# Kernel tuning notes

Hardware: AMD Instinct MI355X
Metric: run time of the kernel (lower is better)

## Reference

```python
import jax, jax.numpy as jnp
import numpy as np

N, E, DIN, DH, DP = 100000, 1600000, 128, 128, 64
BN_EPS = 1e-5


def setup_inputs() -> dict:
    key = jax.random.key(0)
    ks = jax.random.split(key, 24)

    def lin(k, fan_in, shape):
        return jax.random.normal(k, shape, jnp.float32) / np.sqrt(fan_in)

    inp = {
        "x": jax.random.normal(ks[0], (N, DIN), jnp.float32),
        "edge_index": jax.random.randint(ks[1], (2, E), 0, N, dtype=jnp.int32),
        "edge_type": jax.random.randint(ks[2], (E,), 0, 2, dtype=jnp.int32),
        "edge_weight": jax.random.uniform(ks[3], (E,), jnp.float32),
        "seed_node_id": 12345,
        # feature transform
        "ft_w": lin(ks[4], DIN, (DIN, DH)),
        "ft_b": jnp.zeros((DH,), jnp.float32),
        # GCN block 0: 2 layers, stacked along axis 0
        "g0_w": lin(ks[5], DH, (2, DH, DH)),
        "g0_b": jnp.zeros((2, DH), jnp.float32),
        "g0_gamma": jnp.ones((2, DH), jnp.float32),
        "g0_beta": jnp.zeros((2, DH), jnp.float32),
        "g0_rm": 0.1 * jax.random.normal(ks[6], (2, DH), jnp.float32),
        "g0_rv": 0.5 + jax.random.uniform(ks[7], (2, DH), jnp.float32),
        # GCN block 1
        "g1_w": lin(ks[8], DH, (2, DH, DH)),
        "g1_b": jnp.zeros((2, DH), jnp.float32),
        "g1_gamma": jnp.ones((2, DH), jnp.float32),
        "g1_beta": jnp.zeros((2, DH), jnp.float32),
        "g1_rm": 0.1 * jax.random.normal(ks[9], (2, DH), jnp.float32),
        "g1_rv": 0.5 + jax.random.uniform(ks[10], (2, DH), jnp.float32),
        # predictor (input = 4*DH)
        "p_w1": lin(ks[11], 4 * DH, (4 * DH, DP)),
        "p_b1": jnp.zeros((DP,), jnp.float32),
        "p_w2": lin(ks[12], DP, (DP, DP)),
        "p_b2": jnp.zeros((DP,), jnp.float32),
        "p_w3": lin(ks[13], DP, (DP, 1)),
        "p_b3": jnp.zeros((1,), jnp.float32),
    }
    return inp


def _gcn_conv(x, src, dst, w_e, W, b):
    # PyG GCNConv: linear transform, add self-loops (weight 1), symmetric norm, scatter-add, bias.
    h = x @ W                                               # [N, DH]
    deg = jax.ops.segment_sum(w_e, dst, num_segments=N) + 1.0
    dis = jax.lax.rsqrt(deg)
    coef = dis[src] * w_e * dis[dst]                        # [E]
    agg = jax.ops.segment_sum(coef[:, None] * h[src], dst, num_segments=N)
    return agg + h * (1.0 / deg)[:, None] + b               # self-loop norm = 1/deg


def _bn_eval(o, gamma, beta, rm, rv):
    return (o - rm) * gamma * jax.lax.rsqrt(rv + BN_EPS) + beta


def _gcn_block(x, src, dst, w_e, W, b, gamma, beta, rm, rv):
    # layer 0: no residual, followed by ReLU (dropout is a no-op in eval)
    h = _bn_eval(_gcn_conv(x, src, dst, w_e, W[0], b[0]), gamma[0], beta[0], rm[0], rv[0])
    h = jax.nn.relu(h)
    # layer 1: residual (in == out)
    h2 = _bn_eval(_gcn_conv(h, src, dst, w_e, W[1], b[1]), gamma[1], beta[1], rm[1], rv[1])
    return h2 + h


def reference(x, edge_index, edge_type, edge_weight, seed_node_id,
              ft_w, ft_b,
              g0_w, g0_b, g0_gamma, g0_beta, g0_rm, g0_rv,
              g1_w, g1_b, g1_gamma, g1_beta, g1_rm, g1_rv,
              p_w1, p_b1, p_w2, p_b2, p_w3, p_b3):
    src, dst = edge_index[0], edge_index[1]
    h = jax.nn.relu(x @ ft_w + ft_b)
    # edge-type masking via zeroed weights (identical math to slicing the edge list)
    w0 = edge_weight * (edge_type == 0).astype(edge_weight.dtype)
    w1 = edge_weight * (edge_type == 1).astype(edge_weight.dtype)
    x0 = _gcn_block(h, src, dst, w0, g0_w, g0_b, g0_gamma, g0_beta, g0_rm, g0_rv)
    x1 = _gcn_block(h, src, dst, w1, g1_w, g1_b, g1_gamma, g1_beta, g1_rm, g1_rv)
    s0 = jnp.broadcast_to(x0[seed_node_id], (N, DH))
    s1 = jnp.broadcast_to(x1[seed_node_id], (N, DH))
    xc = jnp.concatenate([x0, x1, s0, s1], axis=1)          # [N, 4*DH]
    z = jax.nn.relu(xc @ p_w1 + p_b1)
    z = jax.nn.relu(z @ p_w2 + p_b2)
    out = z @ p_w3 + p_b3                                   # [N, 1]
    return out.squeeze(-1)                                  # [N]
```

## Files before the change

kernel.cpp:

```cpp
#include <hip/hip_runtime.h>
#include <hip/hip_bf16.h>
#include <stdint.h>

#define N_NODES 100000

typedef unsigned short us16;
typedef short bf16x8 __attribute__((ext_vector_type(8)));
typedef float f32x4 __attribute__((ext_vector_type(4)));

__device__ __forceinline__ float us2f(us16 u){
  union{ unsigned int i; float f; } x; x.i = ((unsigned int)u) << 16; return x.f;
}
__device__ __forceinline__ us16 f2us(float f){
  union{ float f; unsigned int i; } x; x.f = f;
  unsigned int i = x.i;
  unsigned int r = (i + 0x7FFFu + ((i >> 16) & 1u)) >> 16;
  return (us16)r;
}

__global__ __launch_bounds__(256) void k_init(int* __restrict__ cnt, int n2){
  int i = blockIdx.x*256 + threadIdx.x;
  if (i < n2) cnt[i]=0;
}

__global__ __launch_bounds__(256) void k_cnt(const int* __restrict__ dst,
                                             const int* __restrict__ et,
                                             int* __restrict__ cnt,
                                             int* __restrict__ eofs, int E){
  int e = blockIdx.x*256 + threadIdx.x;
  if (e>=E) return;
  int d = dst[e]; int t = et[e];
  eofs[e] = atomicAdd(&cnt[t*N_NODES + d], 1);
}

__global__ __launch_bounds__(256) void k_scan_reduce(const int* __restrict__ in, int* __restrict__ bsum, int M){
  __shared__ int sd[256];
  int base = blockIdx.x*2048; int t = threadIdx.x;
  int sum = 0;
  #pragma unroll
  for(int i=0;i<8;i++){ int p = base + t*8 + i; if(p<M) sum += in[p]; }
  sd[t]=sum; __syncthreads();
  for(int s=128;s>0;s>>=1){ if(t<s) sd[t]+=sd[t+s]; __syncthreads(); }
  if(t==0) bsum[blockIdx.x]=sd[0];
}
__global__ void k_scan_top(int* __restrict__ bsum, int B){
  if (threadIdx.x==0){ int run=0; for(int i=0;i<B;i++){ int v=bsum[i]; bsum[i]=run; run+=v; } }
}
__global__ __launch_bounds__(256) void k_scan_apply(const int* __restrict__ in, const int* __restrict__ bsum,
                                                    int* __restrict__ out, int M){
  __shared__ int sd[256];
  int base = blockIdx.x*2048; int t = threadIdx.x;
  int loc[8]; int sum=0;
  #pragma unroll
  for(int i=0;i<8;i++){ int p = base + t*8 + i; int v = (p<M)?in[p]:0; loc[i]=sum; sum+=v; }
  sd[t]=sum; __syncthreads();
  for(int ofs=1;ofs<256;ofs<<=1){
    int v = (t>=ofs)? sd[t-ofs] : 0;
    __syncthreads();
    sd[t]+=v;
    __syncthreads();
  }
  int excl = ((t==0)?0:sd[t-1]) + bsum[blockIdx.x];
  #pragma unroll
  for(int i=0;i<8;i++){ int p = base + t*8 + i; if(p<M) out[p]=excl+loc[i]; }
}

__global__ __launch_bounds__(256) void k_coef(uint2* __restrict__ csr,
                                              const int* __restrict__ rp,
                                              const float* __restrict__ disA, int E){
  int e = blockIdx.x*256+threadIdx.x;
  if(e>=E) return;
  int rpN = rp[N_NODES];
  int t = (e >= rpN) ? 1 : 0;
  uint2 q = csr[e];
  float w = __uint_as_float(q.y) * disA[t*N_NODES + (int)q.x];
  csr[e] = make_uint2(q.x, __float_as_uint(w));
}

__global__ __launch_bounds__(256) void k_prepw(const float* __restrict__ ft_w,
                                               const float* __restrict__ g0_w, const float* __restrict__ g1_w,
                                               const float* __restrict__ p_w1, const float* __restrict__ p_w2,
                                               us16* __restrict__ wt){
  int m = blockIdx.y;
  const float* srcp; int K, NCc; us16* dstp;
  switch(m){
    case 0: srcp=ft_w;        K=128; NCc=128; dstp=wt;        break;
    case 1: srcp=g0_w;        K=128; NCc=128; dstp=wt+16384;  break;
    case 2: srcp=g0_w+16384;  K=128; NCc=128; dstp=wt+32768;  break;
    case 3: srcp=g1_w;        K=128; NCc=128; dstp=wt+49152;  break;
    case 4: srcp=g1_w+16384;  K=128; NCc=128; dstp=wt+65536;  break;
    case 5: srcp=p_w1;        K=256; NCc=64;  dstp=wt+81920;  break;
    default:srcp=p_w2;        K=64;  NCc=64;  dstp=wt+98304;  break;
  }
  int idx = blockIdx.x*256+threadIdx.x;
  if(idx >= K*NCc) return;
  int nn = idx / K, k = idx - nn*K;
  dstp[idx] = f2us(srcp[(size_t)k*NCc + nn]);
}

template<int NC, typename AT>
__device__ __forceinline__ void mgemm_body(int bid,
                 const AT* __restrict__ A0, const AT* __restrict__ A1,
                 int lda, const us16* __restrict__ Wt,
                 const float* __restrict__ bias, const float* __restrict__ addv,
                 us16* __restrict__ C, int ldc, int n, int KC, int relu,
                 us16* Alds, us16* Wlds){
  constexpr int NB = NC/16;
  const int tid = threadIdx.x;
  const int lane = tid & 63, wid = tid >> 6;
  const int rowBase = bid*128;
  f32x4 zero = {0.f,0.f,0.f,0.f};
  f32x4 acc[2][NB];
  #pragma unroll
  for(int m=0;m<2;m++)
    #pragma unroll
    for(int nb=0;nb<NB;nb++) acc[m][nb] = zero;

  for(int kk=0; kk<KC; kk+=64){
    const AT* Ab = (kk<128)? A0 : A1;
    const int kc = (kk<128)? kk : (kk-128);
    #pragma unroll
    for(int p=0;p<4;p++){
      int idx = p*256 + tid;
      int r = idx>>3, u = idx&7;
      int row = rowBase + r;
      uint4 v = make_uint4(0u,0u,0u,0u);
      if(row<n){
        if constexpr (sizeof(AT)==2){
          v = *(const uint4*)(Ab + (size_t)row*lda + kc + u*8);
        } else {
          float4 f0 = *(const float4*)(Ab + (size_t)row*lda + kc + u*8);
          float4 f1 = *(const float4*)(Ab + (size_t)row*lda + kc + u*8 + 4);
          us16 tmp[8] = {f2us(f0.x),f2us(f0.y),f2us(f0.z),f2us(f0.w),
                         f2us(f1.x),f2us(f1.y),f2us(f1.z),f2us(f1.w)};
          v = *(const uint4*)tmp;
        }
      }
      *(uint4*)&Alds[(r*8 + (u ^ (r&7)))*8] = v;
    }
    #pragma unroll
    for(int p=0;p<NB/2;p++){
      int idx = p*256 + tid;
      int cI = idx>>3, u = idx&7;
      uint4 v = *(const uint4*)(Wt + (size_t)cI*KC + kk + u*8);
      *(uint4*)&Wlds[(cI*8 + (u ^ (cI&7)))*8] = v;
    }
    __syncthreads();
    #pragma unroll
    for(int ks=0;ks<2;ks++){
      bf16x8 af[2];
      #pragma unroll
      for(int m=0;m<2;m++){
        int r = wid*32 + m*16 + (lane&15);
        int u = (ks*4 + (lane>>4)) ^ (r&7);
        af[m] = *(const bf16x8*)&Alds[(r*8+u)*8];
      }
      #pragma unroll
      for(int nb=0;nb<NB;nb++){
        int c2 = nb*16 + (lane&15);
        int u = (ks*4 + (lane>>4)) ^ (c2&7);
        bf16x8 bfv = *(const bf16x8*)&Wlds[(c2*8+u)*8];
        #pragma unroll
        for(int m=0;m<2;m++)
          acc[m][nb] = __builtin_amdgcn_mfma_f32_16x16x32_bf16(af[m], bfv, acc[m][nb], 0,0,0);
      }
    }
    __syncthreads();
  }
  #pragma unroll
  for(int nb=0;nb<NB;nb++){
    int col = nb*16 + (lane&15);
    float badd = (bias? bias[col]:0.f) + (addv? addv[col]:0.f);
    #pragma unroll
    for(int m=0;m<2;m++){
      #pragma unroll
      for(int j=0;j<4;j++){
        int row = rowBase + wid*32 + m*16 + (lane>>4)*4 + j;
        if(row<n){
          float v = acc[m][nb][j] + badd;
          if(relu) v = fmaxf(v,0.f);
          C[(size_t)row*ldc + col] = f2us(v);
        }
      }
    }
  }
}

template<int NC, typename AT>
__global__ __launch_bounds__(256) void k_mgemm(const AT* __restrict__ A0, const AT* __restrict__ A1,
                 int lda, const us16* __restrict__ Wt,
                 const float* __restrict__ bias, const float* __restrict__ addv,
                 us16* __restrict__ C, int ldc, int n, int KC, int relu){
  __shared__ us16 smem[128*64 + NC*64];
  mgemm_body<NC,AT>(blockIdx.x, A0,A1,lda, Wt, bias,addv, C,ldc, n,KC,relu, smem, smem+128*64);
}

__global__ __launch_bounds__(256) void k_fill_ft(
    const int* __restrict__ src, const int* __restrict__ dst,
    const int* __restrict__ et, const float* __restrict__ ew,
    const int* __restrict__ rp, const int* __restrict__ eofs,
    uint2* __restrict__ csr, int E, int CB,
    const float* __restrict__ x, const us16* __restrict__ wt_ft, const float* __restrict__ ft_b,
    us16* __restrict__ B0, int n){
  __shared__ us16 smem[128*64 + 128*64];
  int b = blockIdx.x;
  if (b < CB){
    int e = b*256 + threadIdx.x;
    if (e < E){
      int s=src[e], d=dst[e], t=et[e]; float w=ew[e];
      int idx = t*N_NODES + d;
      int pos = rp[idx] + eofs[e];
      csr[pos] = make_uint2((unsigned)s, __float_as_uint(w));
    }
  } else {
    mgemm_body<128,float>(b - CB, x, x, 128, wt_ft, ft_b, nullptr, B0, 128, n, 128, 1,
                          smem, smem + 128*64);
  }
}

__global__ __launch_bounds__(256) void k_deg_l0(
    const uint2* __restrict__ csr, const int* __restrict__ rp, const int* __restrict__ cnt,
    float* __restrict__ disA, int M, int DB, int GB,
    const us16* __restrict__ B0,
    const us16* __restrict__ wt_g00, const us16* __restrict__ wt_g10,
    us16* __restrict__ B1, us16* __restrict__ B2, int n){
  __shared__ us16 smem[128*64 + 128*64];
  int b = blockIdx.x;
  if (b < DB){
    int i = b*256 + threadIdx.x;
    if (i < M){
      int e0 = rp[i], c = cnt[i];
      float s = 1.0f;
      for(int e=e0; e<e0+c; e++) s += __uint_as_float(csr[e].y);
      disA[i] = rsqrtf(s);
    }
  } else if (b < DB + GB){
    mgemm_body<128,us16>(b - DB, B0, B0, 128, wt_g00, nullptr, nullptr, B1, 128, n, 128, 0,
                         smem, smem + 128*64);
  } else {
    mgemm_body<128,us16>(b - DB - GB, B0, B0, 128, wt_g10, nullptr, nullptr, B2, 128, n, 128, 0,
                         smem, smem + 128*64);
  }
}

__global__ __launch_bounds__(256) void k_gemm2(int GB,
    const us16* __restrict__ Aa, const us16* __restrict__ Wa, us16* __restrict__ Ca,
    const us16* __restrict__ Ab, const us16* __restrict__ Wb, us16* __restrict__ Cb, int n){
  __shared__ us16 smem[128*64 + 128*64];
  int b = blockIdx.x;
  if (b < GB)
    mgemm_body<128,us16>(b, Aa, Aa, 128, Wa, nullptr, nullptr, Ca, 128, n, 128, 0, smem, smem+128*64);
  else
    mgemm_body<128,us16>(b-GB, Ab, Ab, 128, Wb, nullptr, nullptr, Cb, 128, n, 128, 0, smem, smem+128*64);
}

__device__ __forceinline__ void agg_body(int bid, const us16* __restrict__ T,
  const uint2* __restrict__ csr,
  const int* __restrict__ rp, const int* __restrict__ cnt, int rowOfs,
  const float* __restrict__ dis,
  const float* __restrict__ bias, const float* __restrict__ gamma, const float* __restrict__ beta,
  const float* __restrict__ rm, const float* __restrict__ rv,
  const us16* __restrict__ resid,
  us16* __restrict__ out, int relu, int n){
  const int wid = threadIdx.x >> 6, lane = threadIdx.x & 63;
  const int qg = lane >> 4;
  const int sl = lane & 15;
  int r = bid*16 + wid*4 + qg;
  if (r >= n) return;
  const int c0 = sl*8;
  int idx = rowOfs + r;
  int e0 = rp[idx];
  int ec = cnt[idx];
  const uint2* cp = csr + e0;
  float a[8];
  #pragma unroll
  for(int j=0;j<8;j++) a[j]=0.f;
  int nchunk = ec >> 2;
  int rem = ec & 3;
  for(int ch=0; ch<nchunk; ch++){
    uint2 q[4];
    #pragma unroll
    for(int i=0;i<4;i++) q[i] = cp[i];
    cp += 4;
    uint4 v[4];
    #pragma unroll
    for(int i=0;i<4;i++) v[i] = *(const uint4*)(T + (size_t)q[i].x*128 + c0);
    #pragma unroll
    for(int i=0;i<4;i++){
      float c = __uint_as_float(q[i].y);
      a[0] += c*us2f((us16)(v[i].x & 0xffffu));
      a[1] += c*us2f((us16)(v[i].x >> 16));
      a[2] += c*us2f((us16)(v[i].y & 0xffffu));
      a[3] += c*us2f((us16)(v[i].y >> 16));
      a[4] += c*us2f((us16)(v[i].z & 0xffffu));
      a[5] += c*us2f((us16)(v[i].z >> 16));
      a[6] += c*us2f((us16)(v[i].w & 0xffffu));
      a[7] += c*us2f((us16)(v[i].w >> 16));
    }
  }
  for(int i=0;i<rem;i++){
    uint2 q = cp[i];
    float c = __uint_as_float(q.y);
    uint4 v = *(const uint4*)(T + (size_t)q.x*128 + c0);
    a[0] += c*us2f((us16)(v.x & 0xffffu));
    a[1] += c*us2f((us16)(v.x >> 16));
    a[2] += c*us2f((us16)(v.y & 0xffffu));
    a[3] += c*us2f((us16)(v.y >> 16));
    a[4] += c*us2f((us16)(v.z & 0xffffu));
    a[5] += c*us2f((us16)(v.z >> 16));
    a[6] += c*us2f((us16)(v.w & 0xffffu));
    a[7] += c*us2f((us16)(v.w >> 16));
  }
  float disr = dis[r]; float invdeg = disr*disr;
  uint4 vs = *(const uint4*)(T + (size_t)r*128 + c0);
  float s[8] = {
    us2f((us16)(vs.x & 0xffffu)), us2f((us16)(vs.x >> 16)),
    us2f((us16)(vs.y & 0xffffu)), us2f((us16)(vs.y >> 16)),
    us2f((us16)(vs.z & 0xffffu)), us2f((us16)(vs.z >> 16)),
    us2f((us16)(vs.w & 0xffffu)), us2f((us16)(vs.w >> 16))
  };
  float4 bi0 = *(const float4*)(bias + c0);
  float4 bi1 = *(const float4*)(bias + c0 + 4);
  float4 ga0 = *(const float4*)(gamma + c0);
  float4 ga1 = *(const float4*)(gamma + c0 + 4);
  float4 be0 = *(const float4*)(beta + c0);
  float4 be1 = *(const float4*)(beta + c0 + 4);
  float4 rm0 = *(const float4*)(rm + c0);
  float4 rm1 = *(const float4*)(rm + c0 + 4);
  float4 rv0 = *(const float4*)(rv + c0);
  float4 rv1 = *(const float4*)(rv + c0 + 4);
  float bif[8] = {bi0.x,bi0.y,bi0.z,bi0.w,bi1.x,bi1.y,bi1.z,bi1.w};
  float gaf[8] = {ga0.x,ga0.y,ga0.z,ga0.w,ga1.x,ga1.y,ga1.z,ga1.w};
  float bef[8] = {be0.x,be0.y,be0.z,be0.w,be1.x,be1.y,be1.z,be1.w};
  float rmf[8] = {rm0.x,rm0.y,rm0.z,rm0.w,rm1.x,rm1.y,rm1.z,rm1.w};
  float rvf[8] = {rv0.x,rv0.y,rv0.z,rv0.w,rv1.x,rv1.y,rv1.z,rv1.w};
  float o[8];
  #pragma unroll
  for(int j=0;j<8;j++){
    float v = a[j]*disr + s[j]*invdeg + bif[j];
    v = (v - rmf[j])*(gaf[j]*rsqrtf(rvf[j] + 1e-5f)) + bef[j];
    if (relu) v = fmaxf(v,0.f);
    o[j] = v;
  }
  if (resid){
    uint4 vr = *(const uint4*)(resid + (size_t)r*128 + c0);
    o[0] += us2f((us16)(vr.x & 0xffffu));
    o[1] += us2f((us16)(vr.x >> 16));
    o[2] += us2f((us16)(vr.y & 0xffffu));
    o[3] += us2f((us16)(vr.y >> 16));
    o[4] += us2f((us16)(vr.z & 0xffffu));
    o[5] += us2f((us16)(vr.z >> 16));
    o[6] += us2f((us16)(vr.w & 0xffffu));
    o[7] += us2f((us16)(vr.w >> 16));
  }
  uint4 up;
  up.x = (unsigned)f2us(o[0]) | ((unsigned)f2us(o[1]) << 16);
  up.y = (unsigned)f2us(o[2]) | ((unsigned)f2us(o[3]) << 16);
  up.z = (unsigned)f2us(o[4]) | ((unsigned)f2us(o[5]) << 16);
  up.w = (unsigned)f2us(o[6]) | ((unsigned)f2us(o[7]) << 16);
  *(uint4*)(out + (size_t)r*128 + c0) = up;
}

__global__ __launch_bounds__(256) void k_agg2(int AB,
  const uint2* __restrict__ csr, const int* __restrict__ rp, const int* __restrict__ cnt,
  const float* __restrict__ disA,
  const us16* __restrict__ Ta,
  const float* __restrict__ ba, const float* __restrict__ gaa, const float* __restrict__ bea,
  const float* __restrict__ rma, const float* __restrict__ rva,
  const us16* __restrict__ resida, us16* __restrict__ outa, int relua,
  const us16* __restrict__ Tb,
  const float* __restrict__ bb, const float* __restrict__ gab, const float* __restrict__ beb,
  const float* __restrict__ rmb, const float* __restrict__ rvb,
  const us16* __restrict__ residb, us16* __restrict__ outb, int relub, int n){
  int b = blockIdx.x;
  if (b < AB)
    agg_body(b, Ta, csr, rp, cnt, 0, disA, ba,gaa,bea,rma,rva, resida, outa, relua, n);
  else
    agg_body(b-AB, Tb, csr, rp, cnt, N_NODES, disA+N_NODES, bb,gab,beb,rmb,rvb, residb, outb, relub, n);
}

__global__ void k_const64(const us16* __restrict__ X0, const us16* __restrict__ X1,
                          const int* __restrict__ seed,
                          const float* __restrict__ pw1, const float* __restrict__ pb1,
                          float* __restrict__ c64){
  int j = threadIdx.x;
  int s = seed[0];
  const us16* x0 = X0 + (size_t)s*128;
  const us16* x1 = X1 + (size_t)s*128;
  float acc = pb1[j];
  #pragma unroll 8
  for(int k=0;k<128;k++) acc += us2f(x0[k]) * pw1[(256+k)*64 + j];
  #pragma unroll 8
  for(int k=0;k<128;k++) acc += us2f(x1[k]) * pw1[(384+k)*64 + j];
  c64[j]=acc;
}

__global__ __launch_bounds__(256) void k_outdot(const us16* __restrict__ Z2, const float* __restrict__ w3,
                                                const float* __restrict__ b3, float* __restrict__ out, int n){
  int r = blockIdx.x*256 + threadIdx.x;
  if(r>=n) return;
  const us16* z = Z2 + (size_t)r*64;
  float acc = b3[0];
  #pragma unroll 8
  for(int j=0;j<64;j++) acc += us2f(z[j])*w3[j];
  out[r]=acc;
}

extern "C" void kernel_launch(void* const* d_in, const int* in_sizes, int n_in,
                              void* d_out, int out_size, void* d_ws, size_t ws_size,
                              hipStream_t stream){
  const int N = N_NODES;
  const int E = in_sizes[2];
  const float* x   = (const float*)d_in[0];
  const int*   ei  = (const int*)d_in[1];
  const int*   et  = (const int*)d_in[2];
  const float* ew  = (const float*)d_in[3];
  const int*   seed= (const int*)d_in[4];
  const float* ft_w= (const float*)d_in[5];
  const float* ft_b= (const float*)d_in[6];
  const float* g0_w= (const float*)d_in[7];
  const float* g0_b= (const float*)d_in[8];
  const float* g0_g= (const float*)d_in[9];
  const float* g0_be=(const float*)d_in[10];
  const float* g0_rm=(const float*)d_in[11];
  const float* g0_rv=(const float*)d_in[12];
  const float* g1_w= (const float*)d_in[13];
  const float* g1_b= (const float*)d_in[14];
  const float* g1_g= (const float*)d_in[15];
  const float* g1_be=(const float*)d_in[16];
  const float* g1_rm=(const float*)d_in[17];
  const float* g1_rv=(const float*)d_in[18];
  const float* p_w1= (const float*)d_in[19];
  const float* p_b1= (const float*)d_in[20];
  const float* p_w2= (const float*)d_in[21];
  const float* p_b2= (const float*)d_in[22];
  const float* p_w3= (const float*)d_in[23];
  const float* p_b3= (const float*)d_in[24];
  float* out = (float*)d_out;

  char* wsp = (char*)d_ws;
  auto alloc = [&](size_t bytes)->char*{ char* p = wsp; wsp += (bytes + 255) & ~(size_t)255; return p; };
  us16* B0 = (us16*)alloc((size_t)N*128*2);
  us16* B1 = (us16*)alloc((size_t)N*128*2);
  us16* B2 = (us16*)alloc((size_t)N*128*2);
  us16* B3 = (us16*)alloc((size_t)N*128*2);
  uint2* csr = (uint2*)alloc((size_t)E*8);
  float* disA=(float*)alloc((size_t)2*N*4);
  int* cnt =(int*)alloc((size_t)2*N*4);
  int* rp  =(int*)alloc((size_t)2*N*4);
  int* bsum=(int*)alloc(4096);
  float* c64=(float*)alloc(256);
  us16* wt =(us16*)alloc((size_t)102400*2);
  int* eofs = (int*)B3;
  us16* Z1 = B1;
  us16* Z2 = B1 + (size_t)N*64;

  const int* srcp = ei;
  const int* dstp = ei + E;

  int M = 2*N;
  int CB = (E+255)/256;
  int GB = (N+127)/128;
  int AB = (N+15)/16;
  int SB = (M+2047)/2048;
  int DB = (M+255)/256;

  k_init<<<(M+255)/256,256,0,stream>>>(cnt,M);
  dim3 pg(64,7);
  k_prepw<<<pg,256,0,stream>>>(ft_w,g0_w,g1_w,p_w1,p_w2,wt);

  const us16* wt_ft = wt;
  const us16* wt_g00= wt+16384;
  const us16* wt_g01= wt+32768;
  const us16* wt_g10= wt+49152;
  const us16* wt_g11= wt+65536;
  const us16* wt_p1 = wt+81920;
  const us16* wt_p2 = wt+98304;

  k_cnt<<<CB,256,0,stream>>>(dstp,et,cnt,eofs,E);
  k_scan_reduce<<<SB,256,0,stream>>>(cnt,bsum,M);
  k_scan_top<<<1,64,0,stream>>>(bsum,SB);
  k_scan_apply<<<SB,256,0,stream>>>(cnt,bsum,rp,M);
  k_fill_ft<<<CB+GB,256,0,stream>>>(srcp,dstp,et,ew,rp,eofs,csr,E,CB, x,wt_ft,ft_b,B0,N);
  k_deg_l0<<<DB+2*GB,256,0,stream>>>(csr,rp,cnt,disA,M,DB,GB, B0,wt_g00,wt_g10,B1,B2,N);
  k_coef<<<(E+255)/256,256,0,stream>>>(csr,rp,disA,E);

  k_agg2<<<2*AB,256,0,stream>>>(AB, csr,rp,cnt,disA,
      B1, g0_b,g0_g,g0_be,g0_rm,g0_rv, nullptr, B0, 1,
      B2, g1_b,g1_g,g1_be,g1_rm,g1_rv, nullptr, B3, 1, N);
  k_gemm2<<<2*GB,256,0,stream>>>(GB, B0,wt_g01,B1, B3,wt_g11,B2, N);
  k_agg2<<<2*AB,256,0,stream>>>(AB, csr,rp,cnt,disA,
      B1, g0_b+128,g0_g+128,g0_be+128,g0_rm+128,g0_rv+128, B0, B0, 0,
      B2, g1_b+128,g1_g+128,g1_be+128,g1_rm+128,g1_rv+128, B3, B3, 0, N);

  k_const64<<<1,64,0,stream>>>(B0,B3,seed,p_w1,p_b1,c64);
  k_mgemm<64,us16><<<GB,256,0,stream>>>(B0,B3,128, wt_p1, nullptr, c64, Z1,64, N,256,1);
  k_mgemm<64,us16><<<GB,256,0,stream>>>(Z1,Z1,64,  wt_p2, p_b2, nullptr, Z2,64, N,64,1);
  k_outdot<<<(N+255)/256,256,0,stream>>>(Z2,p_w3,p_b3,out,N);
}
```

Before: 397.5 us.

## Fuse predictor layer-2 GEMM with output dot; regroup CSR build kernels

Adds a kernel that runs the second predictor GEMM with MFMA and, in the same kernel, applies bias, ReLU and the final 64-wide dot product with a cross-lane shuffle reduction. This removes the Z2 intermediate write and read and one launch. It also reorders the graph-preprocessing launches: the feature-transform GEMM runs standalone first, edge fill and degree computation become separate kernels, and edge coefficient scaling is merged with the layer-0 GEMMs instead of the degree pass. The regrouping changes which work overlaps within a launch and adds one launch to the preprocessing sequence.

After: 392.0 us. No clear change (-1.4%).

```diff
diff --git a/kernel.cpp b/kernel.cpp
--- a/kernel.cpp
+++ b/kernel.cpp
@@ -65,16 +65,27 @@
   for(int i=0;i<8;i++){ int p = base + t*8 + i; if(p<M) out[p]=excl+loc[i]; }
 }
 
-__global__ __launch_bounds__(256) void k_coef(uint2* __restrict__ csr,
-                                              const int* __restrict__ rp,
-                                              const float* __restrict__ disA, int E){
+__global__ __launch_bounds__(256) void k_edge_fill(const int* __restrict__ src, const int* __restrict__ dst,
+  const int* __restrict__ et, const float* __restrict__ ew,
+  const int* __restrict__ rp, const int* __restrict__ eofs,
+  uint2* __restrict__ csr, int E){
   int e = blockIdx.x*256+threadIdx.x;
   if(e>=E) return;
-  int rpN = rp[N_NODES];
-  int t = (e >= rpN) ? 1 : 0;
-  uint2 q = csr[e];
-  float w = __uint_as_float(q.y) * disA[t*N_NODES + (int)q.x];
-  csr[e] = make_uint2(q.x, __float_as_uint(w));
+  int s=src[e], d=dst[e], t=et[e]; float w=ew[e];
+  int idx = t*N_NODES + d;
+  int pos = rp[idx] + eofs[e];
+  csr[pos] = make_uint2((unsigned)s, __float_as_uint(w));
+}
+
+__global__ __launch_bounds__(256) void k_deg_csr(const uint2* __restrict__ csr,
+                                                 const int* __restrict__ rp, const int* __restrict__ cnt,
+                                                 float* __restrict__ disA, int M){
+  int i = blockIdx.x*256+threadIdx.x;
+  if(i>=M) return;
+  int e0 = rp[i], c = cnt[i];
+  float s = 1.0f;
+  for(int e=e0; e<e0+c; e++) s += __uint_as_float(csr[e].y);
+  disA[i] = rsqrtf(s);
 }
 
 __global__ __launch_bounds__(256) void k_prepw(const float* __restrict__ ft_w,
@@ -195,50 +206,28 @@
   mgemm_body<NC,AT>(blockIdx.x, A0,A1,lda, Wt, bias,addv, C,ldc, n,KC,relu, smem, smem+128*64);
 }
 
-__global__ __launch_bounds__(256) void k_fill_ft(
-    const int* __restrict__ src, const int* __restrict__ dst,
-    const int* __restrict__ et, const float* __restrict__ ew,
-    const int* __restrict__ rp, const int* __restrict__ eofs,
-    uint2* __restrict__ csr, int E, int CB,
-    const float* __restrict__ x, const us16* __restrict__ wt_ft, const float* __restrict__ ft_b,
-    us16* __restrict__ B0, int n){
-  __shared__ us16 smem[128*64 + 128*64];
-  int b = blockIdx.x;
-  if (b < CB){
-    int e = b*256 + threadIdx.x;
-    if (e < E){
-      int s=src[e], d=dst[e], t=et[e]; float w=ew[e];
-      int idx = t*N_NODES + d;
-      int pos = rp[idx] + eofs[e];
-      csr[pos] = make_uint2((unsigned)s, __float_as_uint(w));
-    }
-  } else {
-    mgemm_body<128,float>(b - CB, x, x, 128, wt_ft, ft_b, nullptr, B0, 128, n, 128, 1,
-                          smem, smem + 128*64);
-  }
-}
-
-__global__ __launch_bounds__(256) void k_deg_l0(
-    const uint2* __restrict__ csr, const int* __restrict__ rp, const int* __restrict__ cnt,
-    float* __restrict__ disA, int M, int DB, int GB,
+__global__ __launch_bounds__(256) void k_coef_l0(
+    uint2* __restrict__ csr, const int* __restrict__ rp, const float* __restrict__ disA,
+    int E, int EB, int GB,
     const us16* __restrict__ B0,
     const us16* __restrict__ wt_g00, const us16* __restrict__ wt_g10,
     us16* __restrict__ B1, us16* __restrict__ B2, int n){
   __shared__ us16 smem[128*64 + 128*64];
   int b = blockIdx.x;
-  if (b < DB){
-    int i = b*256 + threadIdx.x;
-    if (i < M){
-      int e0 = rp[i], c = cnt[i];
-      float s = 1.0f;
-      for(int e=e0; e<e0+c; e++) s += __uint_as_float(csr[e].y);
-      disA[i] = rsqrtf(s);
-    }
-  } else if (b < DB + GB){
-    mgemm_body<128,us16>(b - DB, B0, B0, 128, wt_g00, nullptr, nullptr, B1, 128, n, 128, 0,
+  if (b < EB){
+    int e = b*256 + threadIdx.x;
+    if (e < E){
+      int rpN = rp[N_NODES];
+      int t = (e >= rpN) ? 1 : 0;
+      uint2 q = csr[e];
+      float w = __uint_as_float(q.y) * disA[t*N_NODES + (int)q.x];
+      csr[e] = make_uint2(q.x, __float_as_uint(w));
+    }
+  } else if (b < EB + GB){
+    mgemm_body<128,us16>(b - EB, B0, B0, 128, wt_g00, nullptr, nullptr, B1, 128, n, 128, 0,
                          smem, smem + 128*64);
   } else {
-    mgemm_body<128,us16>(b - DB - GB, B0, B0, 128, wt_g10, nullptr, nullptr, B2, 128, n, 128, 0,
+    mgemm_body<128,us16>(b - EB - GB, B0, B0, 128, wt_g10, nullptr, nullptr, B2, 128, n, 128, 0,
                          smem, smem + 128*64);
   }
 }
@@ -252,6 +241,90 @@
     mgemm_body<128,us16>(b, Aa, Aa, 128, Wa, nullptr, nullptr, Ca, 128, n, 128, 0, smem, smem+128*64);
   else
     mgemm_body<128,us16>(b-GB, Ab, Ab, 128, Wb, nullptr, nullptr, Cb, 128, n, 128, 0, smem, smem+128*64);
+}
+
+__global__ __launch_bounds__(256) void k_p2out(const us16* __restrict__ Z1,
+                 const us16* __restrict__ Wt, const float* __restrict__ b2,
+                 const float* __restrict__ w3, const float* __restrict__ b3,
+                 float* __restrict__ out, int n){
+  __shared__ us16 smem[128*64 + 64*64];
+  us16* Alds = smem; us16* Wlds = smem + 128*64;
+  const int tid = threadIdx.x;
+  const int lane = tid & 63, wid = tid >> 6;
+  const int rowBase = blockIdx.x*128;
+  f32x4 zero = {0.f,0.f,0.f,0.f};
+  f32x4 acc[2][4];
+  #pragma unroll
+  for(int m=0;m<2;m++)
+    #pragma unroll
+    for(int nb=0;nb<4;nb++) acc[m][nb] = zero;
+
+  {
+    #pragma unroll
+    for(int p=0;p<4;p++){
+      int idx = p*256 + tid;
+      int r = idx>>3, u = idx&7;
+      int row = rowBase + r;
+      uint4 v = make_uint4(0u,0u,0u,0u);
+      if(row<n) v = *(const uint4*)(Z1 + (size_t)row*64 + u*8);
+      *(uint4*)&Alds[(r*8 + (u ^ (r&7)))*8] = v;
+    }
+    #pragma unroll
+    for(int p=0;p<2;p++){
+      int idx = p*256 + tid;
+      int cI = idx>>3, u = idx&7;
+      uint4 v = *(const uint4*)(Wt + (size_t)cI*64 + u*8);
+      *(uint4*)&Wlds[(cI*8 + (u ^ (cI&7)))*8] = v;
+    }
+    __syncthreads();
+    #pragma unroll
+    for(int ks=0;ks<2;ks++){
+      bf16x8 af[2];
+      #pragma unroll
+      for(int m=0;m<2;m++){
+        int r = wid*32 + m*16 + (lane&15);
+        int u = (ks*4 + (lane>>4)) ^ (r&7);
+        af[m] = *(const bf16x8*)&Alds[(r*8+u)*8];
+      }
+      #pragma unroll
+      for(int nb=0;nb<4;nb++){
+        int c2 = nb*16 + (lane&15);
+        int u = (ks*4 + (lane>>4)) ^ (c2&7);
+        bf16x8 bfv = *(const bf16x8*)&Wlds[(c2*8+u)*8];
+        #pragma unroll
+        for(int m=0;m<2;m++)
+          acc[m][nb] = __builtin_amdgcn_mfma_f32_16x16x32_bf16(af[m], bfv, acc[m][nb], 0,0,0);
+      }
+    }
+    __syncthreads();
+  }
+  float w3f[4], b2f[4];
+  #pragma unroll
+  for(int nb=0;nb<4;nb++){
+    int col = nb*16 + (lane&15);
+    w3f[nb] = w3[col];
+    b2f[nb] = b2[col];
+  }
+  float b3v = b3[0];
+  #pragma unroll
+  for(int m=0;m<2;m++){
+    #pragma unroll
+    for(int j=0;j<4;j++){
+      float p = 0.f;
+      #pragma unroll
+      for(int nb=0;nb<4;nb++){
+        float v = acc[m][nb][j] + b2f[nb];
+        v = fmaxf(v, 0.f);
+        p += v * w3f[nb];
+      }
+      p += __shfl_xor(p, 1, 64);
+      p += __shfl_xor(p, 2, 64);
+      p += __shfl_xor(p, 4, 64);
+      p += __shfl_xor(p, 8, 64);
+      int row = rowBase + wid*32 + m*16 + (lane>>4)*4 + j;
+      if ((lane & 15) == 0 && row < n) out[row] = p + b3v;
+    }
+  }
 }
 
 __device__ __forceinline__ void agg_body(int bid, const us16* __restrict__ T,
@@ -393,17 +466,6 @@
   #pragma unroll 8
   for(int k=0;k<128;k++) acc += us2f(x1[k]) * pw1[(384+k)*64 + j];
   c64[j]=acc;
-}
-
-__global__ __launch_bounds__(256) void k_outdot(const us16* __restrict__ Z2, const float* __restrict__ w3,
-                                                const float* __restrict__ b3, float* __restrict__ out, int n){
-  int r = blockIdx.x*256 + threadIdx.x;
-  if(r>=n) return;
-  const us16* z = Z2 + (size_t)r*64;
-  float acc = b3[0];
-  #pragma unroll 8
-  for(int j=0;j<64;j++) acc += us2f(z[j])*w3[j];
-  out[r]=acc;
 }
 
 extern "C" void kernel_launch(void* const* d_in, const int* in_sizes, int n_in,
@@ -453,7 +515,6 @@
   us16* wt =(us16*)alloc((size_t)102400*2);
   int* eofs = (int*)B3;
   us16* Z1 = B1;
-  us16* Z2 = B1 + (size_t)N*64;
 
   const int* srcp = ei;
   const int* dstp = ei + E;
@@ -463,7 +524,6 @@
   int GB = (N+127)/128;
   int AB = (N+15)/16;
   int SB = (M+2047)/2048;
-  int DB = (M+255)/256;
 
   k_init<<<(M+255)/256,256,0,stream>>>(cnt,M);
   dim3 pg(64,7);
@@ -477,13 +537,14 @@
   const us16* wt_p1 = wt+81920;
   const us16* wt_p2 = wt+98304;
 
+  k_mgemm<128,float><<<GB,256,0,stream>>>(x,x,128, wt_ft, ft_b, nullptr, B0,128, N,128,1);
   k_cnt<<<CB,256,0,stream>>>(dstp,et,cnt,eofs,E);
   k_scan_reduce<<<SB,256,0,stream>>>(cnt,bsum,M);
   k_scan_top<<<1,64,0,stream>>>(bsum,SB);
   k_scan_apply<<<SB,256,0,stream>>>(cnt,bsum,rp,M);
-  k_fill_ft<<<CB+GB,256,0,stream>>>(srcp,dstp,et,ew,rp,eofs,csr,E,CB, x,wt_ft,ft_b,B0,N);
-  k_deg_l0<<<DB+2*GB,256,0,stream>>>(csr,rp,cnt,disA,M,DB,GB, B0,wt_g00,wt_g10,B1,B2,N);
-  k_coef<<<(E+255)/256,256,0,stream>>>(csr,rp,disA,E);
+  k_edge_fill<<<CB,256,0,stream>>>(srcp,dstp,et,ew,rp,eofs,csr,E);
+  k_deg_csr<<<(M+255)/256,256,0,stream>>>(csr,rp,cnt,disA,M);
+  k_coef_l0<<<CB+2*GB,256,0,stream>>>(csr,rp,disA,E,CB,GB, B0,wt_g00,wt_g10,B1,B2,N);
 
   k_agg2<<<2*AB,256,0,stream>>>(AB, csr,rp,cnt,disA,
       B1, g0_b,g0_g,g0_be,g0_rm,g0_rv, nullptr, B0, 1,
@@ -495,6 +556,5 @@
 
   k_const64<<<1,64,0,stream>>>(B0,B3,seed,p_w1,p_b1,c64);
   k_mgemm<64,us16><<<GB,256,0,stream>>>(B0,B3,128, wt_p1, nullptr, c64, Z1,64, N,256,1);
-  k_mgemm<64,us16><<<GB,256,0,stream>>>(Z1,Z1,64,  wt_p2, p_b2, nullptr, Z2,64, N,64,1);
-  k_outdot<<<(N+255)/256,256,0,stream>>>(Z2,p_w3,p_b3,out,N);
-}
+  k_p2out<<<GB,256,0,stream>>>(Z1, wt_p2, p_b2, p_w3, p_b3, out, N);
+}
```
